# Kernel tuning notes

Measured on AMD Instinct MI355X. Metric: run time of the kernel, lower is better.

## Reference

```python
import jax, jax.numpy as jnp
import numpy as np

PSIZE = 3
PSTRIDE = 3
N = PSIZE * PSTRIDE   # 9 attention tokens
P = PSIZE ** 2        # 9 pixels per token


def setup_inputs() -> dict:
    key = jax.random.key(0)
    k1, k2, k3, k4, k5 = jax.random.split(key, 5)
    B, H, W, C = 8192, 9, 9, 256
    hidden = C // 2
    x = jax.random.normal(k1, (B, H, W, C), dtype=jnp.float32)
    W_fc = jax.random.normal(k2, (hidden, C), dtype=jnp.float32) * (C ** -0.5)
    b_fc = jax.random.normal(k3, (hidden,), dtype=jnp.float32) * 0.01
    block_idx = jax.random.randint(k4, (B,), 0, 1024, dtype=jnp.int32)
    match_vec = jax.random.randint(k5, (1024, 1), 0, 2, dtype=jnp.int32)
    return {"x": x, "W_fc": W_fc, "b_fc": b_fc, "block_idx": block_idx, "match_vec": match_vec}


def reference(x, W_fc, b_fc, block_idx, match_vec):
    B, H, Wd, C = x.shape
    hidden = W_fc.shape[0]
    scale = (hidden * P) ** -0.5

    # [B, pstride, psize, pstride, psize, C] -> patch-major [B, ps, ps, p, p, C]
    xv = x.reshape(B, PSTRIDE, PSIZE, PSTRIDE, PSIZE, C).transpose(0, 1, 3, 2, 4, 5)
    x_fc = xv.reshape(B, N, P, C)

    # linear projection C -> hidden, then flatten pixels: q [B, N, P*hidden]
    q = (jnp.einsum('bnpc,hc->bnph', x_fc, W_fc) + b_fc).reshape(B, N, P * hidden)

    attn = jnp.einsum('bnd,bmd->bnm', q, q) * scale  # [B, N, N]

    # additive mask: -100 on diagonal, zeroed out entirely for matched samples
    base = jnp.where(jnp.eye(N, dtype=bool), jnp.float32(-100.0), jnp.float32(0.0))
    cur_match = match_vec[block_idx].squeeze(-1)  # [B]
    mask = jnp.where(cur_match[:, None, None] == 1, jnp.float32(0.0), base[None])

    attn = jax.nn.softmax(attn + mask, axis=-1)

    v = xv.reshape(B, N, P * C)
    out = attn @ v  # [B, N, P*C]

    out = out.reshape(B, PSTRIDE, PSTRIDE, PSIZE, PSIZE, C)
    out = out.transpose(0, 1, 3, 2, 4, 5).reshape(B, H, Wd, C)
    return out
```

## Files before the change

### kernel.cpp

```cpp
#include <hip/hip_runtime.h>

typedef short short8 __attribute__((ext_vector_type(8)));
typedef float floatx16 __attribute__((ext_vector_type(16)));
typedef float floatx4 __attribute__((ext_vector_type(4)));

#define ROWS 81
#define CDIM 256
#define XT   0
#define QT   41472
#define SC   66048
#define AB   70144
#define TOT  70656

#define SWX(r) ((((r) & 15) << 4) ^ (((r) & 8) << 3))

__device__ __forceinline__ unsigned short f2bf(float f) {
    union { float f; unsigned int u; } v; v.f = f;
    return (unsigned short)((v.u + 0x7FFFu + ((v.u >> 16) & 1u)) >> 16);
}

__global__ void wconv_kernel(const float* __restrict__ W,
                             unsigned short* __restrict__ Wb, int n) {
    int i = blockIdx.x * 256 + threadIdx.x;
    if (i < n) Wb[i] = f2bf(W[i]);
}

__global__ __launch_bounds__(512, 2)
void attn_kernel(const float* __restrict__ x,
                 const unsigned short* __restrict__ Wb,
                 const float* __restrict__ b_fc,
                 const int* __restrict__ block_idx,
                 const int* __restrict__ match_vec,
                 float* __restrict__ out)
{
    __shared__ __align__(16) char smem[TOT];
    const int b     = blockIdx.x;
    const int t     = threadIdx.x;
    const int lane  = t & 63;
    const int wave  = t >> 6;
    const int l15   = lane & 15;
    const int kg    = lane >> 4;
    const int l31   = lane & 31;
    const int khalf = lane >> 5;

    int cm = 0;
    if (t < 9) cm = match_vec[block_idx[b]];

    short8 wfrag[8];
    {
        const unsigned short* wr = Wb + (wave * 16 + l15) * CDIM + kg * 8;
#pragma unroll
        for (int ks = 0; ks < 8; ++ks)
            wfrag[ks] = *(const short8*)(wr + ks * 32);
    }
    const float bias = b_fc[wave * 16 + l15];

    {
        const float* xb = x + (size_t)b * (ROWS * CDIM);
        for (int k = t; k < ROWS * 32; k += 512) {
            int gr = k >> 5;
            int c0 = (k & 31) * 8;
            float4 a0 = *(const float4*)(xb + gr * CDIM + c0);
            float4 a1 = *(const float4*)(xb + gr * CDIM + c0 + 4);
            int hh = gr / 9, ww = gr - hh * 9;
            int p = (hh % 3) * 3 + (ww % 3);
            int m = (hh / 3) * 3 + (ww / 3);
            int r = p * 9 + m;
            short8 v;
            v[0] = (short)f2bf(a0.x); v[1] = (short)f2bf(a0.y);
            v[2] = (short)f2bf(a0.z); v[3] = (short)f2bf(a0.w);
            v[4] = (short)f2bf(a1.x); v[5] = (short)f2bf(a1.y);
            v[6] = (short)f2bf(a1.z); v[7] = (short)f2bf(a1.w);
            *(short8*)(smem + XT + r * 512 + ((c0 * 2) ^ SWX(r))) = v;
        }
    }
    __syncthreads();

    {
        floatx4 acc[6];
#pragma unroll
        for (int ii = 0; ii < 6; ++ii)
#pragma unroll
            for (int j = 0; j < 4; ++j) acc[ii][j] = 0.f;
#pragma unroll
        for (int ks = 0; ks < 8; ++ks) {
            int cb = ks * 64 + kg * 16;
#pragma unroll
            for (int tile = 0; tile < 6; ++tile) {
                int r = tile * 16 + l15;
                short8 a = *(const short8*)(smem + XT + r * 512 + (cb ^ SWX(r)));
                acc[tile] = __builtin_amdgcn_mfma_f32_16x16x32_bf16(a, wfrag[ks], acc[tile], 0, 0, 0);
            }
        }
        int h2 = (wave * 16 + l15) * 2;
#pragma unroll
        for (int tile = 0; tile < 6; ++tile)
#pragma unroll
            for (int reg = 0; reg < 4; ++reg) {
                int r = tile * 16 + kg * 4 + reg;
                *(unsigned short*)(smem + QT + r * 256 + (h2 ^ ((r & 15) << 4))) =
                    f2bf(acc[tile][reg] + bias);
            }
    }
    __syncthreads();

    if (wave < 4) {
        floatx4 g;
#pragma unroll
        for (int ii = 0; ii < 4; ++ii) g[ii] = 0.f;
        int nc = (l15 < 9) ? l15 : 8;
#pragma unroll
        for (int s = 0; s < 9; ++s) {
            int ks = wave + s * 4;
            int kk = ks * 32 + kg * 8;
            int p  = kk >> 7;
            int h0 = (kk & 127) * 2;
            int row = p * 9 + nc;
            short8 f = *(const short8*)(smem + QT + row * 256 + (h0 ^ ((row & 15) << 4)));
            g = __builtin_amdgcn_mfma_f32_16x16x32_bf16(f, f, g, 0, 0, 0);
        }
        float* sc = (float*)(smem + SC + wave * 1024);
#pragma unroll
        for (int reg = 0; reg < 4; ++reg)
            sc[(kg * 4 + reg) * 16 + l15] = g[reg];
    }
    __syncthreads();

    if (t < 9) {
        const float scale = 0.029462782549439483f;
        const float* sc0 = (const float*)(smem + SC);
        const float* sc1 = (const float*)(smem + SC + 1024);
        const float* sc2 = (const float*)(smem + SC + 2048);
        const float* sc3 = (const float*)(smem + SC + 3072);
        float s[9];
        float mx = -1e30f;
#pragma unroll
        for (int m = 0; m < 9; ++m) {
            int o = t * 16 + m;
            float v = (sc0[o] + sc1[o] + sc2[o] + sc3[o]) * scale;
            if (m == t && cm != 1) v -= 100.f;
            s[m] = v;
            mx = fmaxf(mx, v);
        }
        float sum = 0.f;
#pragma unroll
        for (int m = 0; m < 9; ++m) { s[m] = __expf(s[m] - mx); sum += s[m]; }
        float inv = 1.f / sum;
        unsigned short* ab = (unsigned short*)(smem + AB) + t * 16;
#pragma unroll
        for (int m = 0; m < 9; ++m) ab[m] = f2bf(s[m] * inv);
#pragma unroll
        for (int m = 9; m < 16; ++m) ab[m] = 0;
    }
    __syncthreads();

    {
        const int n  = l31;
        const int nm = (n < 9) ? n : 0;
        short8 bf = *(const short8*)(smem + AB + nm * 32 + khalf * 16);
        floatx16 zero16;
#pragma unroll
        for (int ii = 0; ii < 16; ++ii) zero16[ii] = 0.f;
        float* ob = out + (size_t)b * (ROWS * CDIM);
        int hh = 0, ww = 0;
        if (n < 9) { hh = (n / 3) * 3; ww = (n % 3) * 3; }
#pragma unroll
        for (int tt = 0; tt < 9; ++tt) {
            int tile = wave * 9 + tt;
            int p = tile >> 3;
            int c = (tile & 7) * 32 + l31;
            short8 af;
#pragma unroll
            for (int j = 0; j < 8; ++j) {
                int mm = khalf * 8 + j; if (mm > 8) mm = 8;
                int row = p * 9 + mm;
                af[j] = *(const short*)(smem + XT + row * 512 + ((c * 2) ^ SWX(row)));
            }
            floatx16 dacc = __builtin_amdgcn_mfma_f32_32x32x16_bf16(af, bf, zero16, 0, 0, 0);
            if (n < 9) {
#pragma unroll
                for (int q2 = 0; q2 < 4; ++q2) {
                    int c0 = (tile & 7) * 32 + q2 * 8 + khalf * 4;
                    int gr = (hh + p / 3) * 9 + (ww + p % 3);
                    *(float4*)(ob + gr * CDIM + c0) =
                        make_float4(dacc[q2 * 4 + 0], dacc[q2 * 4 + 1],
                                    dacc[q2 * 4 + 2], dacc[q2 * 4 + 3]);
                }
            }
        }
    }
}

extern "C" void kernel_launch(void* const* d_in, const int* in_sizes, int n_in,
                              void* d_out, int out_size, void* d_ws, size_t ws_size,
                              hipStream_t stream) {
    const float* x    = (const float*)d_in[0];
    const float* W    = (const float*)d_in[1];
    const float* bfc  = (const float*)d_in[2];
    const int*   bidx = (const int*)d_in[3];
    const int*   mvec = (const int*)d_in[4];
    float* outp = (float*)d_out;
    unsigned short* Wb = (unsigned short*)d_ws;

    int nW = in_sizes[1];
    wconv_kernel<<<(nW + 255) / 256, 256, 0, stream>>>(W, Wb, nW);

    int B = in_sizes[0] / (ROWS * CDIM);
    attn_kernel<<<B, 512, 0, stream>>>(x, Wb, bfc, bidx, mvec, outp);
}
```

Measured before the change: 365.5 us.

## Split projection work by row half and hidden pair, use packed bf16 converts

The projection stage is re-partitioned so each wave computes 3 row tiles against two 16-wide hidden slices, reusing each A fragment for two MFMAs instead of loading all six row tiles per wave. Staging now converts fp32 to bf16 with the hardware v_cvt_pk_bf16_f32 instruction instead of software rounding, and the x loads use linear addressing. Launch bounds are raised from 2 to 4 blocks per CU. Some early odd-parity blocks sleep at start to stagger memory traffic. Doubling the per-wave weight fragments under a tighter register budget risks spills, and LDS usage likely still caps occupancy at 2 blocks per CU.

```diff
diff --git a/kernel.cpp b/kernel.cpp
--- a/kernel.cpp
+++ b/kernel.cpp
@@ -19,13 +19,34 @@
     return (unsigned short)((v.u + 0x7FFFu + ((v.u >> 16) & 1u)) >> 16);
 }
 
+__device__ __forceinline__ unsigned int cvtpk(float lo, float hi) {
+    unsigned int r;
+    asm("v_cvt_pk_bf16_f32 %0, %1, %2" : "=v"(r) : "v"(lo), "v"(hi));
+    return r;
+}
+
 __global__ void wconv_kernel(const float* __restrict__ W,
                              unsigned short* __restrict__ Wb, int n) {
     int i = blockIdx.x * 256 + threadIdx.x;
     if (i < n) Wb[i] = f2bf(W[i]);
 }
 
-__global__ __launch_bounds__(512, 2)
+__device__ __forceinline__ void stage_store(char* smem, int k, float4 a0, float4 a1) {
+    int gr = k >> 5;
+    int c0 = (k & 31) * 8;
+    int hh = gr / 9, ww = gr - hh * 9;
+    int p = (hh % 3) * 3 + (ww % 3);
+    int m = (hh / 3) * 3 + (ww / 3);
+    int r = p * 9 + m;
+    uint4 v;
+    v.x = cvtpk(a0.x, a0.y);
+    v.y = cvtpk(a0.z, a0.w);
+    v.z = cvtpk(a1.x, a1.y);
+    v.w = cvtpk(a1.z, a1.w);
+    *(uint4*)(smem + XT + r * 512 + ((c0 * 2) ^ SWX(r))) = v;
+}
+
+__global__ __launch_bounds__(512, 4)
 void attn_kernel(const float* __restrict__ x,
                  const unsigned short* __restrict__ Wb,
                  const float* __restrict__ b_fc,
@@ -43,63 +64,69 @@
     const int l31   = lane & 31;
     const int khalf = lane >> 5;
 
+    if (b < 512 && (((b ^ (b >> 8)) & 1) != 0)) {
+        __builtin_amdgcn_s_sleep(100);
+        __builtin_amdgcn_s_sleep(100);
+    }
+
     int cm = 0;
     if (t < 9) cm = match_vec[block_idx[b]];
 
-    short8 wfrag[8];
-    {
-        const unsigned short* wr = Wb + (wave * 16 + l15) * CDIM + kg * 8;
+    const int rh = (wave & 1) * 48;
+    const int hg = (wave >> 1) * 32;
+
+    short8 wfrag[2][8];
+#pragma unroll
+    for (int s2 = 0; s2 < 2; ++s2) {
+        const unsigned short* wr = Wb + (hg + s2 * 16 + l15) * CDIM + kg * 8;
 #pragma unroll
         for (int ks = 0; ks < 8; ++ks)
-            wfrag[ks] = *(const short8*)(wr + ks * 32);
-    }
-    const float bias = b_fc[wave * 16 + l15];
+            wfrag[s2][ks] = *(const short8*)(wr + ks * 32);
+    }
+    float bias2[2];
+    bias2[0] = b_fc[hg + l15];
+    bias2[1] = b_fc[hg + 16 + l15];
 
     {
         const float* xb = x + (size_t)b * (ROWS * CDIM);
         for (int k = t; k < ROWS * 32; k += 512) {
-            int gr = k >> 5;
-            int c0 = (k & 31) * 8;
-            float4 a0 = *(const float4*)(xb + gr * CDIM + c0);
-            float4 a1 = *(const float4*)(xb + gr * CDIM + c0 + 4);
-            int hh = gr / 9, ww = gr - hh * 9;
-            int p = (hh % 3) * 3 + (ww % 3);
-            int m = (hh / 3) * 3 + (ww / 3);
-            int r = p * 9 + m;
-            short8 v;
-            v[0] = (short)f2bf(a0.x); v[1] = (short)f2bf(a0.y);
-            v[2] = (short)f2bf(a0.z); v[3] = (short)f2bf(a0.w);
-            v[4] = (short)f2bf(a1.x); v[5] = (short)f2bf(a1.y);
-            v[6] = (short)f2bf(a1.z); v[7] = (short)f2bf(a1.w);
-            *(short8*)(smem + XT + r * 512 + ((c0 * 2) ^ SWX(r))) = v;
+            float4 a0 = *(const float4*)(xb + k * 8);
+            float4 a1 = *(const float4*)(xb + k * 8 + 4);
+            stage_store(smem, k, a0, a1);
         }
     }
     __syncthreads();
 
     {
-        floatx4 acc[6];
-#pragma unroll
-        for (int ii = 0; ii < 6; ++ii)
-#pragma unroll
-            for (int j = 0; j < 4; ++j) acc[ii][j] = 0.f;
+        floatx4 acc[3][2];
+#pragma unroll
+        for (int ii = 0; ii < 3; ++ii)
+#pragma unroll
+            for (int s2 = 0; s2 < 2; ++s2)
+#pragma unroll
+                for (int j = 0; j < 4; ++j) acc[ii][s2][j] = 0.f;
 #pragma unroll
         for (int ks = 0; ks < 8; ++ks) {
             int cb = ks * 64 + kg * 16;
 #pragma unroll
-            for (int tile = 0; tile < 6; ++tile) {
-                int r = tile * 16 + l15;
+            for (int tile = 0; tile < 3; ++tile) {
+                int r = rh + tile * 16 + l15;
                 short8 a = *(const short8*)(smem + XT + r * 512 + (cb ^ SWX(r)));
-                acc[tile] = __builtin_amdgcn_mfma_f32_16x16x32_bf16(a, wfrag[ks], acc[tile], 0, 0, 0);
-            }
-        }
-        int h2 = (wave * 16 + l15) * 2;
-#pragma unroll
-        for (int tile = 0; tile < 6; ++tile)
-#pragma unroll
-            for (int reg = 0; reg < 4; ++reg) {
-                int r = tile * 16 + kg * 4 + reg;
-                *(unsigned short*)(smem + QT + r * 256 + (h2 ^ ((r & 15) << 4))) =
-                    f2bf(acc[tile][reg] + bias);
+                acc[tile][0] = __builtin_amdgcn_mfma_f32_16x16x32_bf16(a, wfrag[0][ks], acc[tile][0], 0, 0, 0);
+                acc[tile][1] = __builtin_amdgcn_mfma_f32_16x16x32_bf16(a, wfrag[1][ks], acc[tile][1], 0, 0, 0);
+            }
+        }
+#pragma unroll
+        for (int tile = 0; tile < 3; ++tile)
+#pragma unroll
+            for (int s2 = 0; s2 < 2; ++s2) {
+                int h2 = (hg + s2 * 16 + l15) * 2;
+#pragma unroll
+                for (int reg = 0; reg < 4; ++reg) {
+                    int r = rh + tile * 16 + kg * 4 + reg;
+                    *(unsigned short*)(smem + QT + r * 256 + (h2 ^ ((r & 15) << 4))) =
+                        f2bf(acc[tile][s2][reg] + bias2[s2]);
+                }
             }
     }
     __syncthreads();
```

After: 378.3 us. +3.5%, slower.
